# Kernel optimization log

Hardware: AMD Instinct MI355X
Metric: run time of the kernel (lower is better)

Reference implementation:

```python
import jax, jax.numpy as jnp
import numpy as np

EMBEDDING_DIM = 128
NEG = -1000.0


def setup_inputs() -> dict:
    key = jax.random.key(0)
    ks = jax.random.split(key, 7)
    B, S_src, S_tgt, D = 2, 4096, 512, EMBEDDING_DIM
    return {
        "input_embeddings": jax.random.normal(ks[0], (B, S_src, D), dtype=jnp.float32),
        "token_attention_masks_source": jax.random.randint(ks[1], (B, S_src), 0, 2, dtype=jnp.int32),
        "token_attention_masks_target": jax.random.randint(ks[2], (B, S_tgt), 0, 2, dtype=jnp.int32),
        "encoder_output_embedding": jax.random.normal(ks[3], (B, S_tgt, D), dtype=jnp.float32),
        "w_query": jax.random.uniform(ks[4], (D, D), dtype=jnp.float32),
        "w_key": jax.random.uniform(ks[5], (D, D), dtype=jnp.float32),
        "w_value": jax.random.uniform(ks[6], (D, D), dtype=jnp.float32),
    }


def reference(input_embeddings, token_attention_masks_source,
              token_attention_masks_target, encoder_output_embedding,
              w_query, w_key, w_value):
    # Encoder self-attention branch (attention_type='encoder'), num_heads=1.
    D = w_query.shape[0]
    q = jnp.einsum('bsd,de->bse', input_embeddings, w_query)   # [B,S,D]
    k = jnp.einsum('bsd,de->bse', input_embeddings, w_key)     # [B,S,D]
    v = jnp.einsum('bsd,de->bse', input_embeddings, w_value)   # [B,S,D]
    scores = jnp.einsum('bsd,btd->bst', q, k) / jnp.sqrt(jnp.float32(D))
    # Original adds mask along the QUERY axis: mask[B,S] -> unsqueeze(-1).
    add_mask = jnp.where(token_attention_masks_source == 0, NEG, 0.0).astype(scores.dtype)
    scores = scores + add_mask[:, :, None]
    probs = jax.nn.softmax(scores, axis=2)                      # softmax over keys
    out = jnp.einsum('bst,btd->bsd', probs, v)                  # [B,S,D]
    return out
```

## Files before the change

### kernel.cpp

```cpp
#include <hip/hip_runtime.h>
#include <hip/hip_bf16.h>

#define S_SRC 4096
#define DIM 128
#define BATCH 2
#define NSP 8
#define NQB 32
#define NQG 512

typedef unsigned short u16;
typedef unsigned int u32;
typedef __bf16 bf16x8 __attribute__((ext_vector_type(8)));
typedef float f32x4 __attribute__((ext_vector_type(4)));
typedef u32 u32x4 __attribute__((ext_vector_type(4)));

__device__ __forceinline__ __bf16 bf_hi(float x) { return (__bf16)x; }
__device__ __forceinline__ __bf16 bf_lo(float x, __bf16 h) { return (__bf16)(x - (float)h); }
__device__ __forceinline__ u16 bfu(__bf16 h) { return __builtin_bit_cast(u16, h); }
__device__ __forceinline__ u16 f2bu(float x) { return __builtin_bit_cast(u16, (__bf16)x); }
__device__ __forceinline__ float bu2f(u16 u) { return (float)__builtin_bit_cast(__bf16, u); }
__device__ __forceinline__ u32 pk2(float lo, float hi) {
  return (u32)f2bu(lo) | ((u32)f2bu(hi) << 16);
}
__device__ __forceinline__ void g2l16(const u16* src, u16* ldst) {
  __builtin_amdgcn_global_load_lds((const __attribute__((address_space(1))) void*)src,
                                   (__attribute__((address_space(3))) void*)ldst, 16, 0, 0);
}
#define MFMA __builtin_amdgcn_mfma_f32_16x16x32_bf16

__global__ __launch_bounds__(256) void k_wsplit(const float* __restrict__ wq,
                                                const float* __restrict__ wk,
                                                const float* __restrict__ wv,
                                                u16* __restrict__ wt) {
  int idx = blockIdx.x * 256 + threadIdx.x;
  int mat = idx >> 14;
  int r = idx & 16383;
  int d = r >> 7, e = r & 127;
  const float* w = (mat == 0) ? wq : ((mat == 1) ? wk : wv);
  float x = w[r];
  if (mat == 0) x *= 0.08838834764831845f;
  __bf16 h = bf_hi(x);
  __bf16 l = bf_lo(x, h);
  wt[((mat * 2 + 0) * 128 + e) * 128 + d] = bfu(h);
  wt[((mat * 2 + 1) * 128 + e) * 128 + d] = bfu(l);
}

__global__ __launch_bounds__(256) void k_proj(const float* __restrict__ X,
                                              const u16* __restrict__ wt,
                                              u16* __restrict__ Qh, u16* __restrict__ Ql,
                                              u16* __restrict__ Kh, u16* __restrict__ Kl,
                                              u16* __restrict__ VT) {
  const int mat = blockIdx.x >> 8;
  const int t = blockIdx.x & 255;
  const int b = t >> 7;
  const int tile = t & 127;
  const int tid = threadIdx.x;
  const int w = tid >> 6, lane = tid & 63, g = lane >> 4, l16 = lane & 15;

  bf16x8 a_h[2][4], a_l[2][4];
#pragma unroll
  for (int mf = 0; mf < 2; ++mf) {
    int row = tile * 32 + mf * 16 + l16;
    const float* xr = X + ((size_t)b * S_SRC + row) * DIM;
#pragma unroll
    for (int kf = 0; kf < 4; ++kf) {
      int d0 = kf * 32 + g * 8;
      f32x4 x0 = *(const f32x4*)(xr + d0);
      f32x4 x1 = *(const f32x4*)(xr + d0 + 4);
#pragma unroll
      for (int j = 0; j < 4; ++j) {
        __bf16 h0 = bf_hi(x0[j]);
        __bf16 h1 = bf_hi(x1[j]);
        a_h[mf][kf][j] = h0;
        a_l[mf][kf][j] = bf_lo(x0[j], h0);
        a_h[mf][kf][4 + j] = h1;
        a_l[mf][kf][4 + j] = bf_lo(x1[j], h1);
      }
    }
  }

  const u16* wth = wt + (mat * 2 + 0) * 16384;
  const u16* wtl = wt + (mat * 2 + 1) * 16384;
#pragma unroll
  for (int nf = 0; nf < 2; ++nf) {
    int col = w * 32 + nf * 16 + l16;
    f32x4 acc[2];
    acc[0] = (f32x4){0.f, 0.f, 0.f, 0.f};
    acc[1] = (f32x4){0.f, 0.f, 0.f, 0.f};
#pragma unroll
    for (int kf = 0; kf < 4; ++kf) {
      int d0 = kf * 32 + g * 8;
      bf16x8 bh = *(const bf16x8*)(const void*)(wth + col * 128 + d0);
      bf16x8 bl = *(const bf16x8*)(const void*)(wtl + col * 128 + d0);
#pragma unroll
      for (int mf = 0; mf < 2; ++mf) {
        acc[mf] = MFMA(a_h[mf][kf], bh, acc[mf], 0, 0, 0);
        acc[mf] = MFMA(a_h[mf][kf], bl, acc[mf], 0, 0, 0);
        acc[mf] = MFMA(a_l[mf][kf], bh, acc[mf], 0, 0, 0);
      }
    }
#pragma unroll
    for (int mf = 0; mf < 2; ++mf)
#pragma unroll
      for (int r = 0; r < 4; ++r) {
        int row = tile * 32 + mf * 16 + g * 4 + r;
        float v = acc[mf][r];
        if (mat == 2) {
          VT[((size_t)b * DIM + col) * S_SRC + row] = f2bu(v);
        } else {
          __bf16 h = bf_hi(v);
          __bf16 l = bf_lo(v, h);
          size_t o = ((size_t)b * S_SRC + row) * DIM + col;
          if (mat == 0) { Qh[o] = bfu(h); Ql[o] = bfu(l); }
          else          { Kh[o] = bfu(h); Kl[o] = bfu(l); }
        }
      }
  }
}

__global__ __launch_bounds__(512, 2) void k_attn(const u16* __restrict__ Qh, const u16* __restrict__ Ql,
                                                 const u16* __restrict__ Kh, const u16* __restrict__ Kl,
                                                 const u16* __restrict__ VT,
                                                 float* __restrict__ Pm, float* __restrict__ Pl,
                                                 u16* __restrict__ PO) {
  const int bid = blockIdx.x;
  const int sp = bid & 7;
  const int qb = bid >> 3;
  const int b = qb >> 4;
  const int tid = threadIdx.x;
  const int w = tid >> 6, lane = tid & 63, g = lane >> 4, l16 = lane & 15;

  __shared__ alignas(16) u16 kbuf[2][8192];
  __shared__ alignas(16) u16 vbuf[2][4096];

  const int gr0 = qb * 256 + w * 32;
  bf16x8 q_h[2][4], q_l[2][4];
#pragma unroll
  for (int qg = 0; qg < 2; ++qg) {
    const u16* qph = Qh + ((size_t)gr0 + qg * 16 + l16) * DIM;
    const u16* qpl = Ql + ((size_t)gr0 + qg * 16 + l16) * DIM;
#pragma unroll
    for (int kf = 0; kf < 4; ++kf) {
      int d0 = kf * 32 + g * 8;
      q_h[qg][kf] = *(const bf16x8*)(const void*)(qph + d0);
      q_l[qg][kf] = *(const bf16x8*)(const void*)(qpl + d0);
    }
  }

  f32x4 acc[2][8];
#pragma unroll
  for (int qg = 0; qg < 2; ++qg)
#pragma unroll
    for (int nf = 0; nf < 8; ++nf) acc[qg][nf] = (f32x4){0.f, 0.f, 0.f, 0.f};
  float m0 = -1e30f, m1 = -1e30f, l0 = 0.f, l1 = 0.f;

  const int keys_per = S_SRC / NSP;
  const int key_base = sp * keys_per;
  const int niter = keys_per >> 5;

  const u16* KhB = Kh + (size_t)b * S_SRC * DIM;
  const u16* KlB = Kl + (size_t)b * S_SRC * DIM;
  const u16* VTB = VT + (size_t)b * DIM * S_SRC;

  const int kkey = tid >> 4, kcp = tid & 15;
  const int kcs = (kcp ^ (kkey & 15)) << 3;
  const int vd = tid >> 2, vcp = tid & 3;
  const int vcs = (vcp ^ ((vd >> 1) & 3)) << 3;
  const int wbase = w * 512;

#define STAGE(BUF, KEY0)                                                        \
  {                                                                             \
    g2l16(KhB + ((size_t)((KEY0) + kkey)) * DIM + kcs, &kbuf[BUF][wbase]);      \
    g2l16(KlB + ((size_t)((KEY0) + kkey)) * DIM + kcs, &kbuf[BUF][4096 + wbase]); \
    g2l16(VTB + (size_t)vd * S_SRC + (KEY0) + vcs,     &vbuf[BUF][wbase]);      \
  }

  STAGE(0, key_base)

  const int mg = ((g & 1) << 1) | (g >> 1);
  int cur = 0;
  for (int i = 0; i < niter; ++i) {
    if (i + 1 < niter) {
      STAGE(cur ^ 1, key_base + (i + 1) * 32)
      asm volatile("s_waitcnt vmcnt(3)" ::: "memory");
    } else {
      asm volatile("s_waitcnt vmcnt(0)" ::: "memory");
    }
    __builtin_amdgcn_s_barrier();

    const u16* kb = kbuf[cur];
    f32x4 s00, s01, s10, s11;
    s00 = s01 = s10 = s11 = (f32x4){0.f, 0.f, 0.f, 0.f};
    __builtin_amdgcn_s_setprio(1);
#pragma unroll
    for (int kf = 0; kf < 4; ++kf) {
      int cs = ((kf * 4 + g) ^ l16) << 3;
      bf16x8 kh0 = *(const bf16x8*)(const void*)(kb + l16 * 128 + cs);
      bf16x8 kl0 = *(const bf16x8*)(const void*)(kb + 4096 + l16 * 128 + cs);
      s00 = MFMA(kh0, q_h[0][kf], s00, 0, 0, 0);
      s00 = MFMA(kh0, q_l[0][kf], s00, 0, 0, 0);
      s00 = MFMA(kl0, q_h[0][kf], s00, 0, 0, 0);
      s10 = MFMA(kh0, q_h[1][kf], s10, 0, 0, 0);
      s10 = MFMA(kh0, q_l[1][kf], s10, 0, 0, 0);
      s10 = MFMA(kl0, q_h[1][kf], s10, 0, 0, 0);
      bf16x8 kh1 = *(const bf16x8*)(const void*)(kb + (16 + l16) * 128 + cs);
      bf16x8 kl1 = *(const bf16x8*)(const void*)(kb + 4096 + (16 + l16) * 128 + cs);
      s01 = MFMA(kh1, q_h[0][kf], s01, 0, 0, 0);
      s01 = MFMA(kh1, q_l[0][kf], s01, 0, 0, 0);
      s01 = MFMA(kl1, q_h[0][kf], s01, 0, 0, 0);
      s11 = MFMA(kh1, q_h[1][kf], s11, 0, 0, 0);
      s11 = MFMA(kh1, q_l[1][kf], s11, 0, 0, 0);
      s11 = MFMA(kl1, q_h[1][kf], s11, 0, 0, 0);
    }
    __builtin_amdgcn_s_setprio(0);

    bf16x8 pa0, pa1;
#pragma unroll
    for (int qg = 0; qg < 2; ++qg) {
      f32x4 sA = qg ? s10 : s00;
      f32x4 sB = qg ? s11 : s01;
      float mr = qg ? m1 : m0;
      float lr = qg ? l1 : l0;
      float mx = fmaxf(fmaxf(fmaxf(sA[0], sA[1]), fmaxf(sA[2], sA[3])),
                       fmaxf(fmaxf(sB[0], sB[1]), fmaxf(sB[2], sB[3])));
      mx = fmaxf(mx, __shfl_xor(mx, 16, 64));
      mx = fmaxf(mx, __shfl_xor(mx, 32, 64));
      if (!__all(mx - mr <= 8.0f)) {
        float mn = fmaxf(mr, mx);
        float f = __expf(mr - mn);
        lr *= f;
        mr = mn;
        float fr0 = __shfl(f, g * 4 + 0, 64);
        float fr1 = __shfl(f, g * 4 + 1, 64);
        float fr2 = __shfl(f, g * 4 + 2, 64);
        float fr3 = __shfl(f, g * 4 + 3, 64);
        if (qg == 0) {
#pragma unroll
          for (int nf = 0; nf < 8; ++nf) {
            acc[0][nf][0] *= fr0; acc[0][nf][1] *= fr1;
            acc[0][nf][2] *= fr2; acc[0][nf][3] *= fr3;
          }
        } else {
#pragma unroll
          for (int nf = 0; nf < 8; ++nf) {
            acc[1][nf][0] *= fr0; acc[1][nf][1] *= fr1;
            acc[1][nf][2] *= fr2; acc[1][nf][3] *= fr3;
          }
        }
      }
      float e0 = __expf(sA[0] - mr), e1 = __expf(sA[1] - mr);
      float e2 = __expf(sA[2] - mr), e3 = __expf(sA[3] - mr);
      float e4 = __expf(sB[0] - mr), e5 = __expf(sB[1] - mr);
      float e6 = __expf(sB[2] - mr), e7 = __expf(sB[3] - mr);
      float sm = ((e0 + e1) + (e2 + e3)) + ((e4 + e5) + (e6 + e7));
      sm += __shfl_xor(sm, 16, 64);
      sm += __shfl_xor(sm, 32, 64);
      lr += sm;
      if (qg == 0) { m0 = mr; l0 = lr; } else { m1 = mr; l1 = lr; }

      u32 w0 = pk2(e0, e1), w1 = pk2(e2, e3), w2 = pk2(e4, e5), w3 = pk2(e6, e7);
      u32 x0 = __shfl_xor(w0, 16, 64), x1 = __shfl_xor(w1, 16, 64);
      u32 x2 = __shfl_xor(w2, 16, 64), x3 = __shfl_xor(w3, 16, 64);
      bool odd = (g & 1);
      u32x4 pw;
      pw.x = odd ? x2 : w0;
      pw.y = odd ? x3 : w1;
      pw.z = odd ? w2 : x0;
      pw.w = odd ? w3 : x1;
      if (qg == 0) pa0 = __builtin_bit_cast(bf16x8, pw);
      else         pa1 = __builtin_bit_cast(bf16x8, pw);
    }

    const u16* vb = vbuf[cur];
    __builtin_amdgcn_s_setprio(1);
#pragma unroll
    for (int nf = 0; nf < 8; ++nf) {
      int d = nf * 16 + l16;
      bf16x8 vf = *(const bf16x8*)(const void*)(vb + d * 32 + ((mg ^ ((d >> 1) & 3)) << 3));
      acc[0][nf] = MFMA(pa0, vf, acc[0][nf], 0, 0, 0);
      acc[1][nf] = MFMA(pa1, vf, acc[1][nf], 0, 0, 0);
    }
    __builtin_amdgcn_s_setprio(0);

    __builtin_amdgcn_s_barrier();
    cur ^= 1;
  }

  const int pidx0 = sp * NQG + (gr0 >> 4);
#pragma unroll
  for (int qg = 0; qg < 2; ++qg) {
    u16* po = PO + (size_t)(pidx0 + qg) * 16 * DIM;
#pragma unroll
    for (int nf = 0; nf < 8; ++nf)
#pragma unroll
      for (int r = 0; r < 4; ++r)
        po[(g * 4 + r) * DIM + nf * 16 + l16] = f2bu(acc[qg][nf][r]);
  }
  if (g == 0) { Pm[pidx0 * 16 + l16] = m0; Pl[pidx0 * 16 + l16] = l0; }
  if (g == 1) { Pm[(pidx0 + 1) * 16 + l16] = m1; Pl[(pidx0 + 1) * 16 + l16] = l1; }
#undef STAGE
}

__global__ __launch_bounds__(64) void k_comb(const float* __restrict__ Pm,
                                             const float* __restrict__ Pl,
                                             const u16* __restrict__ PO,
                                             float* __restrict__ out) {
  const int qg = blockIdx.x;
  const int tid = threadIdx.x;

  __shared__ float sc[NSP][16];
  if (tid < 16) {
    float m = -1e30f;
#pragma unroll
    for (int s = 0; s < NSP; ++s) m = fmaxf(m, Pm[(s * NQG + qg) * 16 + tid]);
    float den = 0.f;
#pragma unroll
    for (int s = 0; s < NSP; ++s) {
      float e = __expf(Pm[(s * NQG + qg) * 16 + tid] - m);
      sc[s][tid] = e;
      den += Pl[(s * NQG + qg) * 16 + tid] * e;
    }
    float inv = 1.0f / den;
#pragma unroll
    for (int s = 0; s < NSP; ++s) sc[s][tid] *= inv;
  }
  __syncthreads();

  float* op = out + (size_t)qg * 16 * DIM;
  for (int i = tid; i < 16 * DIM; i += 64) {
    int row = i >> 7;
    float a = 0.f;
#pragma unroll
    for (int s = 0; s < NSP; ++s)
      a += bu2f(PO[(size_t)(s * NQG + qg) * 16 * DIM + i]) * sc[s][row];
    op[i] = a;
  }
}

extern "C" void kernel_launch(void* const* d_in, const int* in_sizes, int n_in,
                              void* d_out, int out_size, void* d_ws, size_t ws_size,
                              hipStream_t stream) {
  const float* X  = (const float*)d_in[0];
  const float* wq = (const float*)d_in[4];
  const float* wk = (const float*)d_in[5];
  const float* wv = (const float*)d_in[6];
  float* out = (float*)d_out;

  u16* WT = (u16*)d_ws;
  u16* Qh = WT + 3 * 2 * 128 * 128;
  u16* Ql = Qh + (size_t)BATCH * S_SRC * DIM;
  u16* Kh = Ql + (size_t)BATCH * S_SRC * DIM;
  u16* Kl = Kh + (size_t)BATCH * S_SRC * DIM;
  u16* VT = Kl + (size_t)BATCH * S_SRC * DIM;
  float* Pm = (float*)(VT + (size_t)BATCH * S_SRC * DIM);
  float* Pl = Pm + (size_t)NSP * NQG * 16;
  u16* PO = (u16*)(Pl + (size_t)NSP * NQG * 16);

  hipLaunchKernelGGL(k_wsplit, dim3(192), dim3(256), 0, stream, wq, wk, wv, WT);
  hipLaunchKernelGGL(k_proj, dim3(3 * 256), dim3(256), 0, stream,
                     X, WT, Qh, Ql, Kh, Kl, VT);
  hipLaunchKernelGGL(k_attn, dim3(NQB * NSP), dim3(512), 0, stream,
                     Qh, Ql, Kh, Kl, VT, Pm, Pl, PO);
  hipLaunchKernelGGL(k_comb, dim3(NQG), dim3(64), 0, stream, Pm, Pl, PO, out);
}
```

Measured before the change: 80.45 us.

## Software-pipeline QK^T of next tile with softmax/PV of current tile; vectorize combine

Restructures the attention loop so the QK^T MFMAs for key tile i+1 are issued before the softmax and PV work of tile i, with a triple-buffered V tile in shared memory and a two-step unrolled loop. The aim is to overlap matrix-core work with the exp/shuffle softmax section and cut idle time between dependent phases. The combine kernel now reads bf16 partials four at a time and writes float4 outputs. The cost is more live registers for the second score set, which could lower occupancy under launch_bounds(512,2), and the loop now waits on all outstanding loads (vmcnt(0)) at each barrier.

```diff
diff --git a/kernel.cpp b/kernel.cpp
--- a/kernel.cpp
+++ b/kernel.cpp
@@ -7,12 +7,14 @@
 #define NSP 8
 #define NQB 32
 #define NQG 512
+#define NITER 16
 
 typedef unsigned short u16;
 typedef unsigned int u32;
 typedef __bf16 bf16x8 __attribute__((ext_vector_type(8)));
 typedef float f32x4 __attribute__((ext_vector_type(4)));
 typedef u32 u32x4 __attribute__((ext_vector_type(4)));
+typedef u16 u16x4 __attribute__((ext_vector_type(4)));
 
 __device__ __forceinline__ __bf16 bf_hi(float x) { return (__bf16)x; }
 __device__ __forceinline__ __bf16 bf_lo(float x, __bf16 h) { return (__bf16)(x - (float)h); }
@@ -118,6 +120,89 @@
   }
 }
 
+__device__ __forceinline__ void qk_tile(const u16* kb, int g, int l16,
+                                        const bf16x8 qh0[4], const bf16x8 ql0[4],
+                                        const bf16x8 qh1[4], const bf16x8 ql1[4],
+                                        f32x4& s00, f32x4& s01, f32x4& s10, f32x4& s11) {
+  s00 = s01 = s10 = s11 = (f32x4){0.f, 0.f, 0.f, 0.f};
+  __builtin_amdgcn_s_setprio(1);
+#pragma unroll
+  for (int kf = 0; kf < 4; ++kf) {
+    int cs = ((kf * 4 + g) ^ l16) << 3;
+    bf16x8 kh0 = *(const bf16x8*)(const void*)(kb + l16 * 128 + cs);
+    bf16x8 kl0 = *(const bf16x8*)(const void*)(kb + 4096 + l16 * 128 + cs);
+    s00 = MFMA(kh0, qh0[kf], s00, 0, 0, 0);
+    s00 = MFMA(kh0, ql0[kf], s00, 0, 0, 0);
+    s00 = MFMA(kl0, qh0[kf], s00, 0, 0, 0);
+    s10 = MFMA(kh0, qh1[kf], s10, 0, 0, 0);
+    s10 = MFMA(kh0, ql1[kf], s10, 0, 0, 0);
+    s10 = MFMA(kl0, qh1[kf], s10, 0, 0, 0);
+    bf16x8 kh1 = *(const bf16x8*)(const void*)(kb + (16 + l16) * 128 + cs);
+    bf16x8 kl1 = *(const bf16x8*)(const void*)(kb + 4096 + (16 + l16) * 128 + cs);
+    s01 = MFMA(kh1, qh0[kf], s01, 0, 0, 0);
+    s01 = MFMA(kh1, ql0[kf], s01, 0, 0, 0);
+    s01 = MFMA(kl1, qh0[kf], s01, 0, 0, 0);
+    s11 = MFMA(kh1, qh1[kf], s11, 0, 0, 0);
+    s11 = MFMA(kh1, ql1[kf], s11, 0, 0, 0);
+    s11 = MFMA(kl1, qh1[kf], s11, 0, 0, 0);
+  }
+  __builtin_amdgcn_s_setprio(0);
+}
+
+__device__ __forceinline__ void sm_pack(f32x4 sA, f32x4 sB, float& mr, float& lr,
+                                        f32x4 acc[8], int g, bf16x8& pa) {
+  float mx = fmaxf(fmaxf(fmaxf(sA[0], sA[1]), fmaxf(sA[2], sA[3])),
+                   fmaxf(fmaxf(sB[0], sB[1]), fmaxf(sB[2], sB[3])));
+  mx = fmaxf(mx, __shfl_xor(mx, 16, 64));
+  mx = fmaxf(mx, __shfl_xor(mx, 32, 64));
+  if (!__all(mx - mr <= 8.0f)) {
+    float mn = fmaxf(mr, mx);
+    float f = __expf(mr - mn);
+    lr *= f;
+    mr = mn;
+    float fr0 = __shfl(f, g * 4 + 0, 64);
+    float fr1 = __shfl(f, g * 4 + 1, 64);
+    float fr2 = __shfl(f, g * 4 + 2, 64);
+    float fr3 = __shfl(f, g * 4 + 3, 64);
+#pragma unroll
+    for (int nf = 0; nf < 8; ++nf) {
+      acc[nf][0] *= fr0; acc[nf][1] *= fr1; acc[nf][2] *= fr2; acc[nf][3] *= fr3;
+    }
+  }
+  float e0 = __expf(sA[0] - mr), e1 = __expf(sA[1] - mr);
+  float e2 = __expf(sA[2] - mr), e3 = __expf(sA[3] - mr);
+  float e4 = __expf(sB[0] - mr), e5 = __expf(sB[1] - mr);
+  float e6 = __expf(sB[2] - mr), e7 = __expf(sB[3] - mr);
+  float sm = ((e0 + e1) + (e2 + e3)) + ((e4 + e5) + (e6 + e7));
+  sm += __shfl_xor(sm, 16, 64);
+  sm += __shfl_xor(sm, 32, 64);
+  lr += sm;
+  u32 w0 = pk2(e0, e1), w1 = pk2(e2, e3), w2 = pk2(e4, e5), w3 = pk2(e6, e7);
+  u32 x0 = __shfl_xor(w0, 16, 64), x1 = __shfl_xor(w1, 16, 64);
+  u32 x2 = __shfl_xor(w2, 16, 64), x3 = __shfl_xor(w3, 16, 64);
+  bool odd = (g & 1);
+  u32x4 pw;
+  pw.x = odd ? x2 : w0;
+  pw.y = odd ? x3 : w1;
+  pw.z = odd ? w2 : x0;
+  pw.w = odd ? w3 : x1;
+  pa = __builtin_bit_cast(bf16x8, pw);
+}
+
+__device__ __forceinline__ void pv_tile(const u16* vb, int mg, int l16,
+                                        bf16x8 pa0, bf16x8 pa1,
+                                        f32x4 acc0[8], f32x4 acc1[8]) {
+  __builtin_amdgcn_s_setprio(1);
+#pragma unroll
+  for (int nf = 0; nf < 8; ++nf) {
+    int d = nf * 16 + l16;
+    bf16x8 vf = *(const bf16x8*)(const void*)(vb + d * 32 + ((mg ^ ((d >> 1) & 3)) << 3));
+    acc0[nf] = MFMA(pa0, vf, acc0[nf], 0, 0, 0);
+    acc1[nf] = MFMA(pa1, vf, acc1[nf], 0, 0, 0);
+  }
+  __builtin_amdgcn_s_setprio(0);
+}
+
 __global__ __launch_bounds__(512, 2) void k_attn(const u16* __restrict__ Qh, const u16* __restrict__ Ql,
                                                  const u16* __restrict__ Kh, const u16* __restrict__ Kl,
                                                  const u16* __restrict__ VT,
@@ -131,33 +216,34 @@
   const int w = tid >> 6, lane = tid & 63, g = lane >> 4, l16 = lane & 15;
 
   __shared__ alignas(16) u16 kbuf[2][8192];
-  __shared__ alignas(16) u16 vbuf[2][4096];
+  __shared__ alignas(16) u16 vbuf[3][4096];
 
   const int gr0 = qb * 256 + w * 32;
-  bf16x8 q_h[2][4], q_l[2][4];
-#pragma unroll
-  for (int qg = 0; qg < 2; ++qg) {
-    const u16* qph = Qh + ((size_t)gr0 + qg * 16 + l16) * DIM;
-    const u16* qpl = Ql + ((size_t)gr0 + qg * 16 + l16) * DIM;
+  bf16x8 qh0[4], ql0[4], qh1[4], ql1[4];
+  {
+    const u16* p0h = Qh + ((size_t)gr0 + l16) * DIM;
+    const u16* p0l = Ql + ((size_t)gr0 + l16) * DIM;
+    const u16* p1h = Qh + ((size_t)gr0 + 16 + l16) * DIM;
+    const u16* p1l = Ql + ((size_t)gr0 + 16 + l16) * DIM;
 #pragma unroll
     for (int kf = 0; kf < 4; ++kf) {
       int d0 = kf * 32 + g * 8;
-      q_h[qg][kf] = *(const bf16x8*)(const void*)(qph + d0);
-      q_l[qg][kf] = *(const bf16x8*)(const void*)(qpl + d0);
-    }
-  }
-
-  f32x4 acc[2][8];
-#pragma unroll
-  for (int qg = 0; qg < 2; ++qg)
-#pragma unroll
-    for (int nf = 0; nf < 8; ++nf) acc[qg][nf] = (f32x4){0.f, 0.f, 0.f, 0.f};
+      qh0[kf] = *(const bf16x8*)(const void*)(p0h + d0);
+      ql0[kf] = *(const bf16x8*)(const void*)(p0l + d0);
+      qh1[kf] = *(const bf16x8*)(const void*)(p1h + d0);
+      ql1[kf] = *(const bf16x8*)(const void*)(p1l + d0);
+    }
+  }
+
+  f32x4 acc0[8], acc1[8];
+#pragma unroll
+  for (int nf = 0; nf < 8; ++nf) {
+    acc0[nf] = (f32x4){0.f, 0.f, 0.f, 0.f};
+    acc1[nf] = (f32x4){0.f, 0.f, 0.f, 0.f};
+  }
   float m0 = -1e30f, m1 = -1e30f, l0 = 0.f, l1 = 0.f;
 
-  const int keys_per = S_SRC / NSP;
-  const int key_base = sp * keys_per;
-  const int niter = keys_per >> 5;
-
+  const int key_base = sp * (S_SRC / NSP);
   const u16* KhB = Kh + (size_t)b * S_SRC * DIM;
   const u16* KlB = Kl + (size_t)b * S_SRC * DIM;
   const u16* VTB = VT + (size_t)b * DIM * S_SRC;
@@ -167,138 +253,75 @@
   const int vd = tid >> 2, vcp = tid & 3;
   const int vcs = (vcp ^ ((vd >> 1) & 3)) << 3;
   const int wbase = w * 512;
-
-#define STAGE(BUF, KEY0)                                                        \
-  {                                                                             \
-    g2l16(KhB + ((size_t)((KEY0) + kkey)) * DIM + kcs, &kbuf[BUF][wbase]);      \
-    g2l16(KlB + ((size_t)((KEY0) + kkey)) * DIM + kcs, &kbuf[BUF][4096 + wbase]); \
-    g2l16(VTB + (size_t)vd * S_SRC + (KEY0) + vcs,     &vbuf[BUF][wbase]);      \
-  }
-
-  STAGE(0, key_base)
-
   const int mg = ((g & 1) << 1) | (g >> 1);
-  int cur = 0;
-  for (int i = 0; i < niter; ++i) {
-    if (i + 1 < niter) {
-      STAGE(cur ^ 1, key_base + (i + 1) * 32)
-      asm volatile("s_waitcnt vmcnt(3)" ::: "memory");
-    } else {
-      asm volatile("s_waitcnt vmcnt(0)" ::: "memory");
-    }
-    __builtin_amdgcn_s_barrier();
-
-    const u16* kb = kbuf[cur];
-    f32x4 s00, s01, s10, s11;
-    s00 = s01 = s10 = s11 = (f32x4){0.f, 0.f, 0.f, 0.f};
-    __builtin_amdgcn_s_setprio(1);
-#pragma unroll
-    for (int kf = 0; kf < 4; ++kf) {
-      int cs = ((kf * 4 + g) ^ l16) << 3;
-      bf16x8 kh0 = *(const bf16x8*)(const void*)(kb + l16 * 128 + cs);
-      bf16x8 kl0 = *(const bf16x8*)(const void*)(kb + 4096 + l16 * 128 + cs);
-      s00 = MFMA(kh0, q_h[0][kf], s00, 0, 0, 0);
-      s00 = MFMA(kh0, q_l[0][kf], s00, 0, 0, 0);
-      s00 = MFMA(kl0, q_h[0][kf], s00, 0, 0, 0);
-      s10 = MFMA(kh0, q_h[1][kf], s10, 0, 0, 0);
-      s10 = MFMA(kh0, q_l[1][kf], s10, 0, 0, 0);
-      s10 = MFMA(kl0, q_h[1][kf], s10, 0, 0, 0);
-      bf16x8 kh1 = *(const bf16x8*)(const void*)(kb + (16 + l16) * 128 + cs);
-      bf16x8 kl1 = *(const bf16x8*)(const void*)(kb + 4096 + (16 + l16) * 128 + cs);
-      s01 = MFMA(kh1, q_h[0][kf], s01, 0, 0, 0);
-      s01 = MFMA(kh1, q_l[0][kf], s01, 0, 0, 0);
-      s01 = MFMA(kl1, q_h[0][kf], s01, 0, 0, 0);
-      s11 = MFMA(kh1, q_h[1][kf], s11, 0, 0, 0);
-      s11 = MFMA(kh1, q_l[1][kf], s11, 0, 0, 0);
-      s11 = MFMA(kl1, q_h[1][kf], s11, 0, 0, 0);
-    }
-    __builtin_amdgcn_s_setprio(0);
-
-    bf16x8 pa0, pa1;
-#pragma unroll
-    for (int qg = 0; qg < 2; ++qg) {
-      f32x4 sA = qg ? s10 : s00;
-      f32x4 sB = qg ? s11 : s01;
-      float mr = qg ? m1 : m0;
-      float lr = qg ? l1 : l0;
-      float mx = fmaxf(fmaxf(fmaxf(sA[0], sA[1]), fmaxf(sA[2], sA[3])),
-                       fmaxf(fmaxf(sB[0], sB[1]), fmaxf(sB[2], sB[3])));
-      mx = fmaxf(mx, __shfl_xor(mx, 16, 64));
-      mx = fmaxf(mx, __shfl_xor(mx, 32, 64));
-      if (!__all(mx - mr <= 8.0f)) {
-        float mn = fmaxf(mr, mx);
-        float f = __expf(mr - mn);
-        lr *= f;
-        mr = mn;
-        float fr0 = __shfl(f, g * 4 + 0, 64);
-        float fr1 = __shfl(f, g * 4 + 1, 64);
-        float fr2 = __shfl(f, g * 4 + 2, 64);
-        float fr3 = __shfl(f, g * 4 + 3, 64);
-        if (qg == 0) {
-#pragma unroll
-          for (int nf = 0; nf < 8; ++nf) {
-            acc[0][nf][0] *= fr0; acc[0][nf][1] *= fr1;
-            acc[0][nf][2] *= fr2; acc[0][nf][3] *= fr3;
-          }
-        } else {
-#pragma unroll
-          for (int nf = 0; nf < 8; ++nf) {
-            acc[1][nf][0] *= fr0; acc[1][nf][1] *= fr1;
-            acc[1][nf][2] *= fr2; acc[1][nf][3] *= fr3;
-          }
-        }
-      }
-      float e0 = __expf(sA[0] - mr), e1 = __expf(sA[1] - mr);
-      float e2 = __expf(sA[2] - mr), e3 = __expf(sA[3] - mr);
-      float e4 = __expf(sB[0] - mr), e5 = __expf(sB[1] - mr);
-      float e6 = __expf(sB[2] - mr), e7 = __expf(sB[3] - mr);
-      float sm = ((e0 + e1) + (e2 + e3)) + ((e4 + e5) + (e6 + e7));
-      sm += __shfl_xor(sm, 16, 64);
-      sm += __shfl_xor(sm, 32, 64);
-      lr += sm;
-      if (qg == 0) { m0 = mr; l0 = lr; } else { m1 = mr; l1 = lr; }
-
-      u32 w0 = pk2(e0, e1), w1 = pk2(e2, e3), w2 = pk2(e4, e5), w3 = pk2(e6, e7);
-      u32 x0 = __shfl_xor(w0, 16, 64), x1 = __shfl_xor(w1, 16, 64);
-      u32 x2 = __shfl_xor(w2, 16, 64), x3 = __shfl_xor(w3, 16, 64);
-      bool odd = (g & 1);
-      u32x4 pw;
-      pw.x = odd ? x2 : w0;
-      pw.y = odd ? x3 : w1;
-      pw.z = odd ? w2 : x0;
-      pw.w = odd ? w3 : x1;
-      if (qg == 0) pa0 = __builtin_bit_cast(bf16x8, pw);
-      else         pa1 = __builtin_bit_cast(bf16x8, pw);
-    }
-
-    const u16* vb = vbuf[cur];
-    __builtin_amdgcn_s_setprio(1);
-#pragma unroll
-    for (int nf = 0; nf < 8; ++nf) {
-      int d = nf * 16 + l16;
-      bf16x8 vf = *(const bf16x8*)(const void*)(vb + d * 32 + ((mg ^ ((d >> 1) & 3)) << 3));
-      acc[0][nf] = MFMA(pa0, vf, acc[0][nf], 0, 0, 0);
-      acc[1][nf] = MFMA(pa1, vf, acc[1][nf], 0, 0, 0);
-    }
-    __builtin_amdgcn_s_setprio(0);
-
-    __builtin_amdgcn_s_barrier();
-    cur ^= 1;
+
+#define STAGE(KB, VB, KEY0)                                                       \
+  {                                                                               \
+    g2l16(KhB + ((size_t)((KEY0) + kkey)) * DIM + kcs, &kbuf[KB][wbase]);         \
+    g2l16(KlB + ((size_t)((KEY0) + kkey)) * DIM + kcs, &kbuf[KB][4096 + wbase]);  \
+    g2l16(VTB + (size_t)vd * S_SRC + (KEY0) + vcs,     &vbuf[VB][wbase]);         \
+  }
+#define WAITBAR { asm volatile("s_waitcnt vmcnt(0)" ::: "memory"); __builtin_amdgcn_s_barrier(); }
+
+  f32x4 a00, a01, a10, a11;
+  f32x4 b00, b01, b10, b11;
+  bf16x8 pa0, pa1;
+
+  STAGE(0, 0, key_base)
+  STAGE(1, 1, key_base + 32)
+  asm volatile("s_waitcnt vmcnt(3)" ::: "memory");
+  __builtin_amdgcn_s_barrier();
+  qk_tile(kbuf[0], g, l16, qh0, ql0, qh1, ql1, a00, a01, a10, a11);
+  WAITBAR
+
+  int va = 0;
+  for (int ii = 0; ii < NITER - 2; ii += 2) {
+    const int v1 = (va + 1) % 3, v2 = (va + 2) % 3;
+    STAGE(ii & 1, v2, key_base + (ii + 2) * 32)
+    qk_tile(kbuf[(ii & 1) ^ 1], g, l16, qh0, ql0, qh1, ql1, b00, b01, b10, b11);
+    sm_pack(a00, a01, m0, l0, acc0, g, pa0);
+    sm_pack(a10, a11, m1, l1, acc1, g, pa1);
+    pv_tile(vbuf[va], mg, l16, pa0, pa1, acc0, acc1);
+    WAITBAR
+    STAGE((ii & 1) ^ 1, va, key_base + (ii + 3) * 32)
+    qk_tile(kbuf[ii & 1], g, l16, qh0, ql0, qh1, ql1, a00, a01, a10, a11);
+    sm_pack(b00, b01, m0, l0, acc0, g, pa0);
+    sm_pack(b10, b11, m1, l1, acc1, g, pa1);
+    pv_tile(vbuf[v1], mg, l16, pa0, pa1, acc0, acc1);
+    WAITBAR
+    va = v2;
+  }
+
+  {
+    const int v1 = (va + 1) % 3;
+    qk_tile(kbuf[1], g, l16, qh0, ql0, qh1, ql1, b00, b01, b10, b11);
+    sm_pack(a00, a01, m0, l0, acc0, g, pa0);
+    sm_pack(a10, a11, m1, l1, acc1, g, pa1);
+    pv_tile(vbuf[va], mg, l16, pa0, pa1, acc0, acc1);
+    sm_pack(b00, b01, m0, l0, acc0, g, pa0);
+    sm_pack(b10, b11, m1, l1, acc1, g, pa1);
+    pv_tile(vbuf[v1], mg, l16, pa0, pa1, acc0, acc1);
   }
 
   const int pidx0 = sp * NQG + (gr0 >> 4);
-#pragma unroll
-  for (int qg = 0; qg < 2; ++qg) {
-    u16* po = PO + (size_t)(pidx0 + qg) * 16 * DIM;
+  {
+    u16* po = PO + (size_t)pidx0 * 16 * DIM;
 #pragma unroll
     for (int nf = 0; nf < 8; ++nf)
 #pragma unroll
       for (int r = 0; r < 4; ++r)
-        po[(g * 4 + r) * DIM + nf * 16 + l16] = f2bu(acc[qg][nf][r]);
+        po[(g * 4 + r) * DIM + nf * 16 + l16] = f2bu(acc0[nf][r]);
+    u16* po1 = PO + (size_t)(pidx0 + 1) * 16 * DIM;
+#pragma unroll
+    for (int nf = 0; nf < 8; ++nf)
+#pragma unroll
+      for (int r = 0; r < 4; ++r)
+        po1[(g * 4 + r) * DIM + nf * 16 + l16] = f2bu(acc1[nf][r]);
   }
   if (g == 0) { Pm[pidx0 * 16 + l16] = m0; Pl[pidx0 * 16 + l16] = l0; }
   if (g == 1) { Pm[(pidx0 + 1) * 16 + l16] = m1; Pl[(pidx0 + 1) * 16 + l16] = l1; }
 #undef STAGE
+#undef WAITBAR
 }
 
 __global__ __launch_bounds__(64) void k_comb(const float* __restrict__ Pm,
@@ -327,13 +350,19 @@
   __syncthreads();
 
   float* op = out + (size_t)qg * 16 * DIM;
-  for (int i = tid; i < 16 * DIM; i += 64) {
-    int row = i >> 7;
-    float a = 0.f;
-#pragma unroll
-    for (int s = 0; s < NSP; ++s)
-      a += bu2f(PO[(size_t)(s * NQG + qg) * 16 * DIM + i]) * sc[s][row];
-    op[i] = a;
+  for (int i = tid; i < 16 * DIM / 4; i += 64) {
+    int row = (i * 4) >> 7;
+    f32x4 a = (f32x4){0.f, 0.f, 0.f, 0.f};
+#pragma unroll
+    for (int s = 0; s < NSP; ++s) {
+      u16x4 p = *(const u16x4*)(const void*)(PO + (size_t)(s * NQG + qg) * 16 * DIM + i * 4);
+      float wgt = sc[s][row];
+      a[0] += bu2f(p.x) * wgt;
+      a[1] += bu2f(p.y) * wgt;
+      a[2] += bu2f(p.z) * wgt;
+      a[3] += bu2f(p.w) * wgt;
+    }
+    *(f32x4*)(op + i * 4) = a;
   }
 }
 
```

Measured after the change: 75.20 us. 6.5% less time.
